# Kernel optimization log

Hardware: AMD Instinct MI355X
Metric: run time of the kernel (lower is better)

Reference implementation:

```python
import jax, jax.numpy as jnp
import numpy as np
from jax import lax

# SLIC superpixel segmentation (skimage-style k-means in 5D color+space feature space).
# The original torch module delegates to skimage.segmentation.slic per image on CPU;
# here we implement the same core algorithm, vectorized:
#   features = [y * m/S, x * m/S, r, g, b]  with S = sqrt(H*W/K), m = compactness
#   iterate: assign each pixel to nearest center (L2), update centers as cluster means.
# Note: we compute dense [HW, K] distances instead of skimage's 2S local window, and we
# skip the RGB->Lab conversion; the clustering math is otherwise the same.

N_SEGMENTS = 100
COMPACTNESS = 10.0
N_ITER = 10


def _slic_single(img):
    H, W, C = img.shape
    K = N_SEGMENTS
    S = (H * W / K) ** 0.5            # grid interval
    ratio = COMPACTNESS / S           # spatial scaling

    yy, xx = jnp.meshgrid(jnp.arange(H, dtype=img.dtype),
                          jnp.arange(W, dtype=img.dtype), indexing='ij')
    feats = jnp.concatenate([(yy * ratio)[..., None], (xx * ratio)[..., None], img],
                            axis=-1).reshape(H * W, C + 2)  # [HW, 5]

    # initialize centers on a regular grid (g x g == K)
    g = int(round(K ** 0.5))
    cy = np.floor((np.arange(g) + 0.5) * H / g).astype(np.int32)
    cx = np.floor((np.arange(g) + 0.5) * W / g).astype(np.int32)
    gy, gx = np.meshgrid(cy, cx, indexing='ij')
    init_idx = jnp.asarray((gy * W + gx).reshape(-1))  # [K]
    centers = feats[init_idx]                          # [K, 5]

    f_sq = jnp.sum(feats * feats, axis=1)              # [HW]

    def assign(centers):
        # squared L2 distances pixel->center: [HW, K]
        d = (f_sq[:, None] + jnp.sum(centers * centers, axis=1)[None, :]
             - 2.0 * jnp.einsum('nf,kf->nk', feats, centers))
        return jnp.argmin(d, axis=1)

    def body(centers, _):
        labels = assign(centers)
        sums = jax.ops.segment_sum(feats, labels, num_segments=K)          # [K, 5]
        counts = jax.ops.segment_sum(jnp.ones((H * W,), feats.dtype), labels,
                                     num_segments=K)                        # [K]
        new_centers = jnp.where(counts[:, None] > 0,
                                sums / jnp.maximum(counts, 1.0)[:, None],
                                centers)
        return new_centers, None

    centers, _ = lax.scan(body, centers, None, length=N_ITER)
    labels = assign(centers)                              # [HW]
    mean_img = centers[labels, 2:2 + C].reshape(H, W, C)  # superpixel-mean image
    return labels.reshape(H, W).astype(jnp.int32), mean_img


def setup_inputs() -> dict:
    key = jax.random.key(0)
    batch_images = jax.random.uniform(key, (8, 224, 224, 3), dtype=jnp.float32)
    return {"batch_images": batch_images}


def reference(batch_images):
    labels, mean_img = jax.vmap(_slic_single)(batch_images)
    return labels, mean_img
```

## Files before the change

kernel.cpp:

```cpp
#include <hip/hip_runtime.h>
#include <math.h>


#pragma clang fp contract(off)

#define BATCH 8
#define HH 224
#define WW 224
#define HWPIX (HH * WW)
#define KSEG 100
#define TPX 512
#define NTILE 98
#define NITER 10
#define UCH 1024
#define UPITCH (UCH + 4)

__device__ __forceinline__ float get_ratio() {
    double S = sqrt((double)(HH * WW) / (double)KSEG);
    return (float)(10.0 / S);
}

__global__ void k_init(const float* __restrict__ img, float* __restrict__ centers) {
#pragma clang fp contract(off)
    int b = blockIdx.x;
    int k = threadIdx.x;
    if (k >= KSEG) return;
    int i = k / 10, j = k % 10;
    int y = (int)floor(((i + 0.5) * (double)HH) / 10.0);
    int x = (int)floor(((j + 0.5) * (double)WW) / 10.0);
    float ratio = get_ratio();
    int n = y * WW + x;
    const float* p = img + ((size_t)b * HWPIX + n) * 3;
    float* c = centers + (b * KSEG + k) * 5;
    c[0] = (float)y * ratio;
    c[1] = (float)x * ratio;
    c[2] = p[0];
    c[3] = p[1];
    c[4] = p[2];
}

__global__ void k_assign(const float* __restrict__ img, const float* __restrict__ centers,
                         float* __restrict__ tileBuf, int* __restrict__ cntT,
                         int* __restrict__ startT, float* __restrict__ outLab,
                         float* __restrict__ outMean, int mode) {
#pragma clang fp contract(off)
    __shared__ float c8[KSEG * 8];
    __shared__ int whist[8 * KSEG];
    __shared__ int tilecnt[KSEG];
    __shared__ int loffs[KSEG];
    __shared__ float wmax[4];
    __shared__ unsigned long long kmask[2];
    int b = blockIdx.y, tile = blockIdx.x, tid = threadIdx.x;
    int lane = tid & 63, w = tid >> 6;

    for (int i = tid; i < KSEG * 5; i += 256) {
        int k = i / 5, f = i - 5 * k;
        c8[k * 8 + f] = centers[(size_t)b * KSEG * 5 + i];
    }
    if (mode == 0)
        for (int i = tid; i < 8 * KSEG; i += 256) whist[i] = 0;
    __syncthreads();
    if (tid < KSEG) {
        const float* ck = c8 + tid * 8;
        float s = ck[0] * ck[0];
        s = s + ck[1] * ck[1];
        s = s + ck[2] * ck[2];
        s = s + ck[3] * ck[3];
        s = s + ck[4] * ck[4];
        c8[tid * 8 + 5] = s;
    }
    __syncthreads();

    float ratio = get_ratio();
    int n0 = tile * TPX + tid;
    float yf[2], xf[2], rr[2], gg[2], bb[2], fsq[2], dmin[2];
    int kb[2];
#pragma unroll
    for (int p = 0; p < 2; ++p) {
        int n = n0 + p * 256;
        int y = n / WW, x = n - y * WW;
        yf[p] = (float)y * ratio;
        xf[p] = (float)x * ratio;
        const float* pp = img + ((size_t)b * HWPIX + n) * 3;
        rr[p] = pp[0]; gg[p] = pp[1]; bb[p] = pp[2];
        float s = yf[p] * yf[p];
        s = s + xf[p] * xf[p];
        s = s + rr[p] * rr[p];
        s = s + gg[p] * gg[p];
        s = s + bb[p] * bb[p];
        fsq[p] = s;
        dmin[p] = INFINITY;
        kb[p] = 0;
    }

#define EVALK(kk)                                                              \
    {                                                                          \
        int k_ = (kk);                                                         \
        float4 v0 = *reinterpret_cast<const float4*>(&c8[k_ * 8]);             \
        float c4v = c8[k_ * 8 + 4];                                            \
        float csqv = c8[k_ * 8 + 5];                                           \
        _Pragma("unroll")                                                      \
        for (int p = 0; p < 2; ++p) {                                          \
            float dot = yf[p] * v0.x;                                          \
            dot = __fmaf_rn(xf[p], v0.y, dot);                                 \
            dot = __fmaf_rn(rr[p], v0.z, dot);                                 \
            dot = __fmaf_rn(gg[p], v0.w, dot);                                 \
            dot = __fmaf_rn(bb[p], c4v, dot);                                  \
            float d = (fsq[p] + csqv) - 2.0f * dot;                            \
            if (d < dmin[p] || (d == dmin[p] && k_ < kb[p])) {                 \
                dmin[p] = d; kb[p] = k_;                                       \
            }                                                                  \
        }                                                                      \
    }

    int y0t = (tile * TPX) / WW, y1t = (tile * TPX + TPX - 1) / WW;
    int rmid = ((y0t + y1t) / 2) * 10 / HH;
    int rlo = (rmid > 0) ? rmid - 1 : 0;
    int rhi = (rmid < 9) ? rmid + 1 : 9;
    int kA0 = rlo * 10, kA1 = rhi * 10 + 10;
    for (int k = kA0; k < kA1; ++k) EVALK(k);

    float tmax = fmaxf(dmin[0], dmin[1]);
    for (int d = 32; d > 0; d >>= 1) tmax = fmaxf(tmax, __shfl_xor(tmax, d));
    if (lane == 0) wmax[w] = tmax;
    __syncthreads();
    float dmaxB = fmaxf(fmaxf(wmax[0], wmax[1]), fmaxf(wmax[2], wmax[3])) + 1.0f;

    {
        bool keep = false;
        if (tid < KSEG) {
            int k = tid;
            bool instat = (k >= kA0 && k < kA1);
            float cyf = c8[k * 8 + 0];
            float t0 = (float)y0t * ratio - cyf;
            float t1 = cyf - (float)y1t * ratio;
            float t = fmaxf(fmaxf(t0, t1), 0.0f);
            keep = (!instat) && (t * t <= dmaxB);
        }
        unsigned long long bm = __ballot(keep);
        if (lane == 0 && w < 2) kmask[w] = bm;
    }
    __syncthreads();

    {
        unsigned long long m0 = kmask[0], m1 = kmask[1];
        while (m0) { int k = __builtin_ctzll(m0); m0 &= m0 - 1; EVALK(k); }
        while (m1) { int k = 64 + __builtin_ctzll(m1); m1 &= m1 - 1; EVALK(k); }
    }
#undef EVALK

    if (mode == 1) {
#pragma unroll
        for (int p = 0; p < 2; ++p) {
            int n = n0 + p * 256;
            outLab[(size_t)b * HWPIX + n] = (float)kb[p];
            float* om = outMean + ((size_t)b * HWPIX + n) * 3;
            om[0] = c8[kb[p] * 8 + 2];
            om[1] = c8[kb[p] * 8 + 3];
            om[2] = c8[kb[p] * 8 + 4];
        }
        return;
    }

    unsigned long long lmask_lt = (lane == 0) ? 0ull : (~0ull >> (64 - lane));
    int rank_w[2], cnt_w[2];
#pragma unroll
    for (int p = 0; p < 2; ++p) {
        unsigned long long todo = __ballot(1);
        while (todo) {
            int leader = __builtin_ctzll(todo);
            int lval = __shfl(kb[p], leader);
            unsigned long long mset = __ballot(kb[p] == lval);
            if (kb[p] == lval) {
                cnt_w[p] = (int)__popcll(mset);
                rank_w[p] = (int)__popcll(mset & lmask_lt);
            }
            todo &= ~mset;
        }
    }
#pragma unroll
    for (int p = 0; p < 2; ++p)
        if (rank_w[p] == 0) whist[(p * 4 + w) * KSEG + kb[p]] = cnt_w[p];
    __syncthreads();
    if (tid < KSEG) {
        int s = 0;
        for (int g = 0; g < 8; ++g) s += whist[g * KSEG + tid];
        tilecnt[tid] = s;
    }
    __syncthreads();
    if (tid < KSEG) {
        int bsum = 0;
        for (int j = 0; j < tid; ++j) bsum += tilecnt[j];
        loffs[tid] = bsum;
        cntT[((size_t)b * KSEG + tid) * NTILE + tile] = tilecnt[tid];
        startT[((size_t)b * KSEG + tid) * NTILE + tile] = bsum;
    }
    __syncthreads();

    float* tb = tileBuf + (size_t)(b * NTILE + tile) * 5 * TPX;
#pragma unroll
    for (int p = 0; p < 2; ++p) {
        int g = p * 4 + w;
        int r = rank_w[p];
        for (int g2 = 0; g2 < g; ++g2) r += whist[g2 * KSEG + kb[p]];
        int pos = loffs[kb[p]] + r;
        tb[0 * TPX + pos] = yf[p];
        tb[1 * TPX + pos] = xf[p];
        tb[2 * TPX + pos] = rr[p];
        tb[3 * TPX + pos] = gg[p];
        tb[4 * TPX + pos] = bb[p];
    }
}

__global__ void k_update(const float* __restrict__ tileBuf, const int* __restrict__ cntT,
                         const int* __restrict__ startT, float* __restrict__ centers) {
#pragma clang fp contract(off)
    __shared__ int srcL[NTILE];
    __shared__ int dstL[NTILE + 1];
    __shared__ float ubuf[5][UPITCH];
    int k = blockIdx.x, b = blockIdx.y, tid = threadIdx.x;
    int lane = tid & 63;

    if (tid < 64) {
        int carry = 0;
        for (int c0 = 0; c0 < NTILE; c0 += 64) {
            int idx = c0 + lane;
            int c = (idx < NTILE) ? cntT[((size_t)b * KSEG + k) * NTILE + idx] : 0;
            int s = (idx < NTILE) ? startT[((size_t)b * KSEG + k) * NTILE + idx] : 0;
            int incl = c;
            for (int d = 1; d < 64; d <<= 1) {
                int t = __shfl_up(incl, d);
                if (lane >= d) incl += t;
            }
            if (idx < NTILE) { srcL[idx] = s; dstL[idx] = carry + incl - c; }
            carry += __shfl(incl, 63);
        }
        if (lane == 0) dstL[NTILE] = carry;
    }
    __syncthreads();
    int total = dstL[NTILE];

    float acc = 0.f;
    for (int c0 = 0; c0 < total; c0 += UCH) {
        int m = min(UCH, total - c0);
        for (int jj = tid; jj < m; jj += 256) {
            int j = c0 + jj;
            int lo = 0, hi = NTILE;
            while (hi - lo > 1) {
                int mid = (lo + hi) >> 1;
                if (dstL[mid] <= j) lo = mid; else hi = mid;
            }
            int src = srcL[lo] + (j - dstL[lo]);
            const float* tb = tileBuf + (size_t)(b * NTILE + lo) * 5 * TPX;
#pragma unroll
            for (int ch = 0; ch < 5; ++ch)
                ubuf[ch][jj] = tb[ch * TPX + src];
        }
        __syncthreads();
        if (tid < 5) {
            float a = acc;
            const float4* bp4 = reinterpret_cast<const float4*>(&ubuf[tid][0]);
            int nf4 = m >> 2;
#pragma unroll 4
            for (int i = 0; i < nf4; ++i) {
                float4 v = bp4[i];
                a = a + v.x;
                a = a + v.y;
                a = a + v.z;
                a = a + v.w;
            }
            for (int i = nf4 << 2; i < m; ++i) a = a + ubuf[tid][i];
            acc = a;
        }
        __syncthreads();
    }
    if (tid < 5 && total > 0) {
        centers[(b * KSEG + k) * 5 + tid] = acc / (float)total;
    }
}

extern "C" void kernel_launch(void* const* d_in, const int* in_sizes, int n_in,
                              void* d_out, int out_size, void* d_ws, size_t ws_size,
                              hipStream_t stream) {
    const float* img = (const float*)d_in[0];
    float* outLab = (float*)d_out;
    float* outMean = outLab + (size_t)BATCH * HWPIX;

    char* ws = (char*)d_ws;
    float* centers = (float*)ws;  ws += (size_t)BATCH * KSEG * 5 * sizeof(float);
    float* tileBuf = (float*)ws;  ws += (size_t)BATCH * NTILE * 5 * TPX * sizeof(float);
    int* cntT      = (int*)ws;    ws += (size_t)BATCH * KSEG * NTILE * sizeof(int);
    int* startT    = (int*)ws;    ws += (size_t)BATCH * KSEG * NTILE * sizeof(int);

    k_init<<<dim3(BATCH), 128, 0, stream>>>(img, centers);
    for (int it = 0; it < NITER; ++it) {
        k_assign<<<dim3(NTILE, BATCH), 256, 0, stream>>>(img, centers, tileBuf, cntT,
                                                         startT, outLab, outMean, 0);
        k_update<<<dim3(KSEG, BATCH), 256, 0, stream>>>(tileBuf, cntT, startT, centers);
    }
    k_assign<<<dim3(NTILE, BATCH), 256, 0, stream>>>(img, centers, tileBuf, cntT,
                                                     startT, outLab, outMean, 1);
}
```

Before: 297.1 us.

## Double assign tile size, stage sorted pixels in LDS, parallelize offset scans

Each assign block now handles 1024 pixels (4 per thread) instead of 512, which halves the tile count seen by the update kernel and lets its per-cluster tile scan run in a single wavefront pass. The per-tile exclusive prefix over cluster counts is now a wave shuffle scan instead of a serial loop per thread. Sorted pixel features are scattered into shared memory first and then written to global memory with a coalesced linear copy, replacing scattered global writes. In exchange there are more registers and shared memory per block and fewer blocks in flight, and the block's center-pruning bound now covers taller tiles, so fewer clusters may be skipped.

New measurement: 322.0 us. 1.08x slower.

```diff
diff --git a/kernel.cpp b/kernel.cpp
--- a/kernel.cpp
+++ b/kernel.cpp
@@ -9,8 +9,8 @@
 #define WW 224
 #define HWPIX (HH * WW)
 #define KSEG 100
-#define TPX 512
-#define NTILE 98
+#define TPX 1024
+#define NTILE 49
 #define NITER 10
 #define UCH 1024
 #define UPITCH (UCH + 4)
@@ -45,11 +45,13 @@
                          float* __restrict__ outMean, int mode) {
 #pragma clang fp contract(off)
     __shared__ float c8[KSEG * 8];
-    __shared__ int whist[8 * KSEG];
+    __shared__ int whist[16 * KSEG];
     __shared__ int tilecnt[KSEG];
     __shared__ int loffs[KSEG];
+    __shared__ float sorted[5][TPX];
     __shared__ float wmax[4];
     __shared__ unsigned long long kmask[2];
+    __shared__ int sum0s;
     int b = blockIdx.y, tile = blockIdx.x, tid = threadIdx.x;
     int lane = tid & 63, w = tid >> 6;
 
@@ -58,7 +60,7 @@
         c8[k * 8 + f] = centers[(size_t)b * KSEG * 5 + i];
     }
     if (mode == 0)
-        for (int i = tid; i < 8 * KSEG; i += 256) whist[i] = 0;
+        for (int i = tid; i < 16 * KSEG; i += 256) whist[i] = 0;
     __syncthreads();
     if (tid < KSEG) {
         const float* ck = c8 + tid * 8;
@@ -73,10 +75,10 @@
 
     float ratio = get_ratio();
     int n0 = tile * TPX + tid;
-    float yf[2], xf[2], rr[2], gg[2], bb[2], fsq[2], dmin[2];
-    int kb[2];
-#pragma unroll
-    for (int p = 0; p < 2; ++p) {
+    float yf[4], xf[4], rr[4], gg[4], bb[4], fsq[4], dmin[4];
+    int kb[4];
+#pragma unroll
+    for (int p = 0; p < 4; ++p) {
         int n = n0 + p * 256;
         int y = n / WW, x = n - y * WW;
         yf[p] = (float)y * ratio;
@@ -100,7 +102,7 @@
         float c4v = c8[k_ * 8 + 4];                                            \
         float csqv = c8[k_ * 8 + 5];                                           \
         _Pragma("unroll")                                                      \
-        for (int p = 0; p < 2; ++p) {                                          \
+        for (int p = 0; p < 4; ++p) {                                          \
             float dot = yf[p] * v0.x;                                          \
             dot = __fmaf_rn(xf[p], v0.y, dot);                                 \
             dot = __fmaf_rn(rr[p], v0.z, dot);                                 \
@@ -120,7 +122,7 @@
     int kA0 = rlo * 10, kA1 = rhi * 10 + 10;
     for (int k = kA0; k < kA1; ++k) EVALK(k);
 
-    float tmax = fmaxf(dmin[0], dmin[1]);
+    float tmax = fmaxf(fmaxf(dmin[0], dmin[1]), fmaxf(dmin[2], dmin[3]));
     for (int d = 32; d > 0; d >>= 1) tmax = fmaxf(tmax, __shfl_xor(tmax, d));
     if (lane == 0) wmax[w] = tmax;
     __syncthreads();
@@ -151,7 +153,7 @@
 
     if (mode == 1) {
 #pragma unroll
-        for (int p = 0; p < 2; ++p) {
+        for (int p = 0; p < 4; ++p) {
             int n = n0 + p * 256;
             outLab[(size_t)b * HWPIX + n] = (float)kb[p];
             float* om = outMean + ((size_t)b * HWPIX + n) * 3;
@@ -163,9 +165,9 @@
     }
 
     unsigned long long lmask_lt = (lane == 0) ? 0ull : (~0ull >> (64 - lane));
-    int rank_w[2], cnt_w[2];
-#pragma unroll
-    for (int p = 0; p < 2; ++p) {
+    int rank_w[4], cnt_w[4];
+#pragma unroll
+    for (int p = 0; p < 4; ++p) {
         unsigned long long todo = __ballot(1);
         while (todo) {
             int leader = __builtin_ctzll(todo);
@@ -179,37 +181,60 @@
         }
     }
 #pragma unroll
-    for (int p = 0; p < 2; ++p)
+    for (int p = 0; p < 4; ++p)
         if (rank_w[p] == 0) whist[(p * 4 + w) * KSEG + kb[p]] = cnt_w[p];
     __syncthreads();
     if (tid < KSEG) {
         int s = 0;
-        for (int g = 0; g < 8; ++g) s += whist[g * KSEG + tid];
+#pragma unroll
+        for (int g = 0; g < 16; ++g) s += whist[g * KSEG + tid];
         tilecnt[tid] = s;
     }
     __syncthreads();
+    if (tid < 64) {
+        int v = tilecnt[tid];
+        int incl = v;
+        for (int d = 1; d < 64; d <<= 1) {
+            int t = __shfl_up(incl, d);
+            if (lane >= d) incl += t;
+        }
+        loffs[tid] = incl - v;
+        if (lane == 63) sum0s = incl;
+    }
+    __syncthreads();
+    if (w == 1) {
+        int i2 = tid;
+        int v = (i2 < KSEG) ? tilecnt[i2] : 0;
+        int incl = v;
+        for (int d = 1; d < 64; d <<= 1) {
+            int t = __shfl_up(incl, d);
+            if (lane >= d) incl += t;
+        }
+        if (i2 < KSEG) loffs[i2] = sum0s + incl - v;
+    }
+    __syncthreads();
     if (tid < KSEG) {
-        int bsum = 0;
-        for (int j = 0; j < tid; ++j) bsum += tilecnt[j];
-        loffs[tid] = bsum;
         cntT[((size_t)b * KSEG + tid) * NTILE + tile] = tilecnt[tid];
-        startT[((size_t)b * KSEG + tid) * NTILE + tile] = bsum;
-    }
-    __syncthreads();
-
-    float* tb = tileBuf + (size_t)(b * NTILE + tile) * 5 * TPX;
-#pragma unroll
-    for (int p = 0; p < 2; ++p) {
+        startT[((size_t)b * KSEG + tid) * NTILE + tile] = loffs[tid];
+    }
+
+#pragma unroll
+    for (int p = 0; p < 4; ++p) {
         int g = p * 4 + w;
         int r = rank_w[p];
         for (int g2 = 0; g2 < g; ++g2) r += whist[g2 * KSEG + kb[p]];
         int pos = loffs[kb[p]] + r;
-        tb[0 * TPX + pos] = yf[p];
-        tb[1 * TPX + pos] = xf[p];
-        tb[2 * TPX + pos] = rr[p];
-        tb[3 * TPX + pos] = gg[p];
-        tb[4 * TPX + pos] = bb[p];
-    }
+        sorted[0][pos] = yf[p];
+        sorted[1][pos] = xf[p];
+        sorted[2][pos] = rr[p];
+        sorted[3][pos] = gg[p];
+        sorted[4][pos] = bb[p];
+    }
+    __syncthreads();
+
+    float* tb = tileBuf + (size_t)(b * NTILE + tile) * 5 * TPX;
+    const float* sflat = &sorted[0][0];
+    for (int i = tid; i < 5 * TPX; i += 256) tb[i] = sflat[i];
 }
 
 __global__ void k_update(const float* __restrict__ tileBuf, const int* __restrict__ cntT,
@@ -222,20 +247,15 @@
     int lane = tid & 63;
 
     if (tid < 64) {
-        int carry = 0;
-        for (int c0 = 0; c0 < NTILE; c0 += 64) {
-            int idx = c0 + lane;
-            int c = (idx < NTILE) ? cntT[((size_t)b * KSEG + k) * NTILE + idx] : 0;
-            int s = (idx < NTILE) ? startT[((size_t)b * KSEG + k) * NTILE + idx] : 0;
-            int incl = c;
-            for (int d = 1; d < 64; d <<= 1) {
-                int t = __shfl_up(incl, d);
-                if (lane >= d) incl += t;
-            }
-            if (idx < NTILE) { srcL[idx] = s; dstL[idx] = carry + incl - c; }
-            carry += __shfl(incl, 63);
-        }
-        if (lane == 0) dstL[NTILE] = carry;
+        int c = (lane < NTILE) ? cntT[((size_t)b * KSEG + k) * NTILE + lane] : 0;
+        int s = (lane < NTILE) ? startT[((size_t)b * KSEG + k) * NTILE + lane] : 0;
+        int incl = c;
+        for (int d = 1; d < 64; d <<= 1) {
+            int t = __shfl_up(incl, d);
+            if (lane >= d) incl += t;
+        }
+        if (lane < NTILE) { srcL[lane] = s; dstL[lane] = incl - c; }
+        if (lane == 63) dstL[NTILE] = incl;
     }
     __syncthreads();
     int total = dstL[NTILE];
```
